# Optimization experiments

Measured on AMD Instinct MI355X. Metric: run time of the kernel, lower is better.

Reference implementation:

```python
import jax, jax.numpy as jnp
import numpy as np

B, T, I, H = 4096, 128, 32, 64


def _u(key, shape, bound):
    return jax.random.uniform(key, shape, jnp.float32, -bound, bound)


def setup_inputs() -> dict:
    key = jax.random.key(0)
    ks = jax.random.split(key, 14)
    bound = 1.0 / np.sqrt(H)  # torch LSTM/Linear default init scale
    inp = {
        "x": jax.random.normal(ks[0], (B, T, I), jnp.float32),
        "Wih0": _u(ks[1], (4 * H, I), bound),
        "Whh0": _u(ks[2], (4 * H, H), bound),
        "bih0": _u(ks[3], (4 * H,), bound),
        "bhh0": _u(ks[4], (4 * H,), bound),
        "Wih1": _u(ks[5], (4 * H, H), bound),
        "Whh1": _u(ks[6], (4 * H, H), bound),
        "bih1": _u(ks[7], (4 * H,), bound),
        "bhh1": _u(ks[8], (4 * H,), bound),
        "Wc1": _u(ks[9], (32, H), 1.0 / np.sqrt(H)),
        "bc1": _u(ks[10], (32,), 1.0 / np.sqrt(H)),
        "Wc2": _u(ks[11], (1, 32), 1.0 / np.sqrt(32)),
        "bc2": _u(ks[12], (1,), 1.0 / np.sqrt(32)),
    }
    return inp


def lstm_layer(x_tbi, Wih, Whh, bih, bhh):
    """x_tbi: [T, B, in]. Returns (all hidden [T,B,H], final hidden [B,H]).
    PyTorch gate order: i, f, g, o."""
    b = x_tbi.shape[1]
    h0 = jnp.zeros((b, Whh.shape[1]), x_tbi.dtype)
    c0 = jnp.zeros_like(h0)
    # precompute input projections for all timesteps in one big GEMM
    xproj = jnp.einsum('tbi,gi->tbg', x_tbi, Wih) + (bih + bhh)

    def step(carry, xp_t):
        h, c = carry
        gates = xp_t + h @ Whh.T  # [B, 4H]
        i, f, g, o = jnp.split(gates, 4, axis=-1)
        c = jax.nn.sigmoid(f) * c + jax.nn.sigmoid(i) * jnp.tanh(g)
        h = jax.nn.sigmoid(o) * jnp.tanh(c)
        return (h, c), h

    (hT, _), hs = jax.lax.scan(step, (h0, c0), xproj)
    return hs, hT


def reference(x, Wih0, Whh0, bih0, bhh0, Wih1, Whh1, bih1, bhh1, Wc1, bc1, Wc2, bc2):
    x_tbi = jnp.transpose(x, (1, 0, 2))  # [T, B, I]
    hs0, _ = lstm_layer(x_tbi, Wih0, Whh0, bih0, bhh0)
    # dropout between layers is identity in eval mode
    _, hT = lstm_layer(hs0, Wih1, Whh1, bih1, bhh1)  # h_n[-1]: [B, H]
    hidden = jax.nn.relu(hT @ Wc1.T + bc1)  # [B, 32]; classifier dropout = identity (eval)
    out = hidden @ Wc2.T + bc2  # [B, 1]
    return out.squeeze(-1)  # [B]
```

## Files before the change

### kernel.cpp

```cpp
#include <hip/hip_runtime.h>


#define TT 128
#define II 32
#define HH 64

typedef _Float16 half8 __attribute__((ext_vector_type(8)));
typedef float floatx4 __attribute__((ext_vector_type(4)));

__device__ __forceinline__ float fsig(float x) {
    return __builtin_amdgcn_rcpf(1.0f + __expf(-x));
}
__device__ __forceinline__ float ftanhf(float x) {
    return 1.0f - 2.0f * __builtin_amdgcn_rcpf(1.0f + __expf(2.0f * x));
}

__device__ __forceinline__ half8 load_w_frag(const float* __restrict__ W, int n, int K, int k0) {
    const float* p = W + (size_t)n * K + k0;
    float4 a = *(const float4*)p;
    float4 b = *(const float4*)(p + 4);
    half8 h;
    h[0] = (_Float16)a.x; h[1] = (_Float16)a.y; h[2] = (_Float16)a.z; h[3] = (_Float16)a.w;
    h[4] = (_Float16)b.x; h[5] = (_Float16)b.y; h[6] = (_Float16)b.z; h[7] = (_Float16)b.w;
    return h;
}

__global__ __launch_bounds__(512, 2) void lstm_fused(
    const float* __restrict__ x,
    const float* __restrict__ Wih0, const float* __restrict__ Whh0,
    const float* __restrict__ bih0, const float* __restrict__ bhh0,
    const float* __restrict__ Wih1, const float* __restrict__ Whh1,
    const float* __restrict__ bih1, const float* __restrict__ bhh1,
    const float* __restrict__ Wc1, const float* __restrict__ bc1,
    const float* __restrict__ Wc2, const float* __restrict__ bc2,
    float* __restrict__ out)
{
    __shared__ __align__(16) _Float16 xs[16][40];
    __shared__ __align__(16) _Float16 h0s[16][72];
    __shared__ __align__(16) _Float16 h1s[16][72];
    __shared__ __align__(16) float h1f[16][68];
    __shared__ float hid[16][32];

    const int tid  = threadIdx.x;
    const int wid  = tid >> 6;
    const int w4   = wid & 3;
    const bool isL0 = (wid < 4);
    const int lane = tid & 63;
    const int q  = lane >> 4;
    const int lr = lane & 15;
    const int b0 = blockIdx.x * 16;

    half8 bx0[4], bh0[4][2];
    half8 bi1[4][2], bh1[4][2];
    float biasv[4];
    if (isL0) {
        #pragma unroll
        for (int g = 0; g < 4; ++g) {
            int n = (w4 + 4 * g) * 16 + lr;
            bx0[g]    = load_w_frag(Wih0, n, 32, q * 8);
            bh0[g][0] = load_w_frag(Whh0, n, 64, q * 8);
            bh0[g][1] = load_w_frag(Whh0, n, 64, 32 + q * 8);
            biasv[g]  = bih0[n] + bhh0[n];
        }
    } else {
        #pragma unroll
        for (int g = 0; g < 4; ++g) {
            int n = (w4 + 4 * g) * 16 + lr;
            bi1[g][0] = load_w_frag(Wih1, n, 64, q * 8);
            bi1[g][1] = load_w_frag(Wih1, n, 64, 32 + q * 8);
            bh1[g][0] = load_w_frag(Whh1, n, 64, q * 8);
            bh1[g][1] = load_w_frag(Whh1, n, 64, 32 + q * 8);
            biasv[g]  = bih1[n] + bhh1[n];
        }
    }

    for (int i = tid; i < 16 * 72; i += 512) {
        ((_Float16*)h0s)[i] = (_Float16)0.0f;
        ((_Float16*)h1s)[i] = (_Float16)0.0f;
    }

    float cr[4] = {0.f, 0.f, 0.f, 0.f};

    const int xm = (tid >> 4) & 15;
    const int xf = (tid & 15) * 2;
    const float* xrow = x + ((size_t)(b0 + xm) * TT) * II + xf;
    float2 xbuf = {0.f, 0.f};
    if (isL0) {
        float2 x0 = *(const float2*)(xrow);
        xs[xm][xf]     = (_Float16)x0.x;
        xs[xm][xf + 1] = (_Float16)x0.y;
        if (TT > 1) xbuf = *(const float2*)(xrow + 1 * II);
    }

    for (int k = 0; k <= TT; ++k) {
        __syncthreads();

        const bool doL0 = isL0 && (k < TT);
        const bool doL1 = (!isL0) && (k >= 1);
        float hnew[4];
        float2 xnew = xbuf;

        if (doL0) {
            half8 xfrag = *(const half8*)&xs[lr][q * 8];
            half8 h0a   = *(const half8*)&h0s[lr][q * 8];
            half8 h0b   = *(const half8*)&h0s[lr][32 + q * 8];
            if (k + 2 < TT) xnew = *(const float2*)(xrow + (size_t)(k + 2) * II);
            floatx4 a0[4];
            #pragma unroll
            for (int g = 0; g < 4; ++g) {
                floatx4 accA = {biasv[g], biasv[g], biasv[g], biasv[g]};
                floatx4 z = {0.f, 0.f, 0.f, 0.f};
                accA = __builtin_amdgcn_mfma_f32_16x16x32_f16(xfrag, bx0[g],    accA, 0, 0, 0);
                accA = __builtin_amdgcn_mfma_f32_16x16x32_f16(h0a,   bh0[g][0], accA, 0, 0, 0);
                floatx4 accB = __builtin_amdgcn_mfma_f32_16x16x32_f16(h0b, bh0[g][1], z, 0, 0, 0);
                a0[g] = accA + accB;
            }
            #pragma unroll
            for (int r = 0; r < 4; ++r) {
                float ig = fsig(a0[0][r]);
                float fg = fsig(a0[1][r]);
                float gg = ftanhf(a0[2][r]);
                float og = fsig(a0[3][r]);
                float c = fg * cr[r] + ig * gg;
                cr[r] = c;
                hnew[r] = og * ftanhf(c);
            }
        }
        if (doL1) {
            half8 g0a = *(const half8*)&h0s[lr][q * 8];
            half8 g0b = *(const half8*)&h0s[lr][32 + q * 8];
            half8 h1a = *(const half8*)&h1s[lr][q * 8];
            half8 h1b = *(const half8*)&h1s[lr][32 + q * 8];
            floatx4 a1[4];
            #pragma unroll
            for (int g = 0; g < 4; ++g) {
                floatx4 accA = {biasv[g], biasv[g], biasv[g], biasv[g]};
                floatx4 z = {0.f, 0.f, 0.f, 0.f};
                accA = __builtin_amdgcn_mfma_f32_16x16x32_f16(g0a, bi1[g][0], accA, 0, 0, 0);
                accA = __builtin_amdgcn_mfma_f32_16x16x32_f16(g0b, bi1[g][1], accA, 0, 0, 0);
                floatx4 accB = __builtin_amdgcn_mfma_f32_16x16x32_f16(h1a, bh1[g][0], z,    0, 0, 0);
                accB         = __builtin_amdgcn_mfma_f32_16x16x32_f16(h1b, bh1[g][1], accB, 0, 0, 0);
                a1[g] = accA + accB;
            }
            #pragma unroll
            for (int r = 0; r < 4; ++r) {
                float ig = fsig(a1[0][r]);
                float fg = fsig(a1[1][r]);
                float gg = ftanhf(a1[2][r]);
                float og = fsig(a1[3][r]);
                float c = fg * cr[r] + ig * gg;
                cr[r] = c;
                hnew[r] = og * ftanhf(c);
            }
        }

        __syncthreads();

        if (doL0) {
            #pragma unroll
            for (int r = 0; r < 4; ++r)
                h0s[q * 4 + r][w4 * 16 + lr] = (_Float16)hnew[r];
            if (k + 1 < TT) {
                xs[xm][xf]     = (_Float16)xbuf.x;
                xs[xm][xf + 1] = (_Float16)xbuf.y;
            }
            xbuf = xnew;
        }
        if (doL1) {
            if (k == TT) {
                #pragma unroll
                for (int r = 0; r < 4; ++r)
                    h1f[q * 4 + r][w4 * 16 + lr] = hnew[r];
            } else {
                #pragma unroll
                for (int r = 0; r < 4; ++r)
                    h1s[q * 4 + r][w4 * 16 + lr] = (_Float16)hnew[r];
            }
        }
    }
    __syncthreads();

    if (tid < 256) {
        int m = tid >> 4;
        int u = (tid & 15) * 2;
        float a = bc1[u], b = bc1[u + 1];
        const float* w0 = Wc1 + u * 64;
        const float* w1 = Wc1 + (u + 1) * 64;
        #pragma unroll 8
        for (int kk = 0; kk < 64; ++kk) {
            float hv = h1f[m][kk];
            a += hv * w0[kk];
            b += hv * w1[kk];
        }
        hid[m][u]     = fmaxf(a, 0.f);
        hid[m][u + 1] = fmaxf(b, 0.f);
    }
    __syncthreads();
    if (tid < 16) {
        float o = bc2[0];
        #pragma unroll
        for (int u = 0; u < 32; ++u) o += hid[tid][u] * Wc2[u];
        out[b0 + tid] = o;
    }
}

extern "C" void kernel_launch(void* const* d_in, const int* in_sizes, int n_in,
                              void* d_out, int out_size, void* d_ws, size_t ws_size,
                              hipStream_t stream) {
    (void)in_sizes; (void)n_in; (void)d_ws; (void)ws_size; (void)out_size;
    const float* x    = (const float*)d_in[0];
    const float* Wih0 = (const float*)d_in[1];
    const float* Whh0 = (const float*)d_in[2];
    const float* bih0 = (const float*)d_in[3];
    const float* bhh0 = (const float*)d_in[4];
    const float* Wih1 = (const float*)d_in[5];
    const float* Whh1 = (const float*)d_in[6];
    const float* bih1 = (const float*)d_in[7];
    const float* bhh1 = (const float*)d_in[8];
    const float* Wc1  = (const float*)d_in[9];
    const float* bc1  = (const float*)d_in[10];
    const float* Wc2  = (const float*)d_in[11];
    const float* bc2  = (const float*)d_in[12];
    lstm_fused<<<dim3(256), dim3(512), 0, stream>>>(
        x, Wih0, Whh0, bih0, bhh0, Wih1, Whh1, bih1, bhh1, Wc1, bc1, Wc2, bc2,
        (float*)d_out);
}
```

Measured before the change: 226.5 us.

## Double-buffer LDS hidden state to drop a barrier and fuse gate activations

Hidden state and x tiles in LDS become ping-pong buffers indexed by step parity, so each timestep needs one __syncthreads instead of two. Gate activations are rewritten to use exp2 directly, and sigmoid(a)*tanh(b) is fused into a single reciprocal with clamping. MFMA accumulation is chained into one accumulator instead of two summed partial chains. The goal is to cut barrier stalls and transcendental count on the serial recurrence, at the cost of more LDS and a longer dependent MFMA chain.

```diff
diff --git a/kernel.cpp b/kernel.cpp
--- a/kernel.cpp
+++ b/kernel.cpp
@@ -8,12 +8,7 @@
 typedef _Float16 half8 __attribute__((ext_vector_type(8)));
 typedef float floatx4 __attribute__((ext_vector_type(4)));
 
-__device__ __forceinline__ float fsig(float x) {
-    return __builtin_amdgcn_rcpf(1.0f + __expf(-x));
-}
-__device__ __forceinline__ float ftanhf(float x) {
-    return 1.0f - 2.0f * __builtin_amdgcn_rcpf(1.0f + __expf(2.0f * x));
-}
+#define LOG2E 1.4426950408889634f
 
 __device__ __forceinline__ half8 load_w_frag(const float* __restrict__ W, int n, int K, int k0) {
     const float* p = W + (size_t)n * K + k0;
@@ -23,6 +18,20 @@
     h[0] = (_Float16)a.x; h[1] = (_Float16)a.y; h[2] = (_Float16)a.z; h[3] = (_Float16)a.w;
     h[4] = (_Float16)b.x; h[5] = (_Float16)b.y; h[6] = (_Float16)b.z; h[7] = (_Float16)b.w;
     return h;
+}
+
+__device__ __forceinline__ float sig_tanh(float a, float b) {
+    float bb = fminf(fmaxf(b, -15.f), 15.f);
+    float u  = __builtin_amdgcn_exp2f(bb * (2.0f * LOG2E));
+    float v  = __builtin_amdgcn_exp2f(-a * LOG2E);
+    float num = u - 1.0f;
+    float d1  = u + 1.0f;
+    float den = fmaf(v, d1, d1);
+    return num * __builtin_amdgcn_rcpf(den);
+}
+
+__device__ __forceinline__ float fsig(float x) {
+    return __builtin_amdgcn_rcpf(1.0f + __builtin_amdgcn_exp2f(-x * LOG2E));
 }
 
 __global__ __launch_bounds__(512, 2) void lstm_fused(
@@ -35,9 +44,9 @@
     const float* __restrict__ Wc2, const float* __restrict__ bc2,
     float* __restrict__ out)
 {
-    __shared__ __align__(16) _Float16 xs[16][40];
-    __shared__ __align__(16) _Float16 h0s[16][72];
-    __shared__ __align__(16) _Float16 h1s[16][72];
+    __shared__ __align__(16) _Float16 xs[2][16][40];
+    __shared__ __align__(16) _Float16 h0s[2][16][72];
+    __shared__ __align__(16) _Float16 h1s[2][16][72];
     __shared__ __align__(16) float h1f[16][68];
     __shared__ float hid[16][32];
 
@@ -74,7 +83,7 @@
         }
     }
 
-    for (int i = tid; i < 16 * 72; i += 512) {
+    for (int i = tid; i < 2 * 16 * 72; i += 512) {
         ((_Float16*)h0s)[i] = (_Float16)0.0f;
         ((_Float16*)h1s)[i] = (_Float16)0.0f;
     }
@@ -87,82 +96,74 @@
     float2 xbuf = {0.f, 0.f};
     if (isL0) {
         float2 x0 = *(const float2*)(xrow);
-        xs[xm][xf]     = (_Float16)x0.x;
-        xs[xm][xf + 1] = (_Float16)x0.y;
+        xs[0][xm][xf]     = (_Float16)x0.x;
+        xs[0][xm][xf + 1] = (_Float16)x0.y;
         if (TT > 1) xbuf = *(const float2*)(xrow + 1 * II);
     }
 
     for (int k = 0; k <= TT; ++k) {
         __syncthreads();
 
+        const int rd = (k + 1) & 1;
+        const int wr = k & 1;
         const bool doL0 = isL0 && (k < TT);
         const bool doL1 = (!isL0) && (k >= 1);
         float hnew[4];
         float2 xnew = xbuf;
 
         if (doL0) {
-            half8 xfrag = *(const half8*)&xs[lr][q * 8];
-            half8 h0a   = *(const half8*)&h0s[lr][q * 8];
-            half8 h0b   = *(const half8*)&h0s[lr][32 + q * 8];
+            half8 xfrag = *(const half8*)&xs[wr][lr][q * 8];
+            half8 h0a   = *(const half8*)&h0s[rd][lr][q * 8];
+            half8 h0b   = *(const half8*)&h0s[rd][lr][32 + q * 8];
             if (k + 2 < TT) xnew = *(const float2*)(xrow + (size_t)(k + 2) * II);
             floatx4 a0[4];
             #pragma unroll
             for (int g = 0; g < 4; ++g) {
-                floatx4 accA = {biasv[g], biasv[g], biasv[g], biasv[g]};
-                floatx4 z = {0.f, 0.f, 0.f, 0.f};
-                accA = __builtin_amdgcn_mfma_f32_16x16x32_f16(xfrag, bx0[g],    accA, 0, 0, 0);
-                accA = __builtin_amdgcn_mfma_f32_16x16x32_f16(h0a,   bh0[g][0], accA, 0, 0, 0);
-                floatx4 accB = __builtin_amdgcn_mfma_f32_16x16x32_f16(h0b, bh0[g][1], z, 0, 0, 0);
-                a0[g] = accA + accB;
+                floatx4 acc = {biasv[g], biasv[g], biasv[g], biasv[g]};
+                acc = __builtin_amdgcn_mfma_f32_16x16x32_f16(xfrag, bx0[g],    acc, 0, 0, 0);
+                acc = __builtin_amdgcn_mfma_f32_16x16x32_f16(h0a,   bh0[g][0], acc, 0, 0, 0);
+                acc = __builtin_amdgcn_mfma_f32_16x16x32_f16(h0b,   bh0[g][1], acc, 0, 0, 0);
+                a0[g] = acc;
             }
             #pragma unroll
             for (int r = 0; r < 4; ++r) {
-                float ig = fsig(a0[0][r]);
-                float fg = fsig(a0[1][r]);
-                float gg = ftanhf(a0[2][r]);
-                float og = fsig(a0[3][r]);
-                float c = fg * cr[r] + ig * gg;
+                float sf = fsig(a0[1][r]);
+                float c  = fmaf(sf, cr[r], sig_tanh(a0[0][r], a0[2][r]));
                 cr[r] = c;
-                hnew[r] = og * ftanhf(c);
+                hnew[r] = sig_tanh(a0[3][r], c);
             }
         }
         if (doL1) {
-            half8 g0a = *(const half8*)&h0s[lr][q * 8];
-            half8 g0b = *(const half8*)&h0s[lr][32 + q * 8];
-            half8 h1a = *(const half8*)&h1s[lr][q * 8];
-            half8 h1b = *(const half8*)&h1s[lr][32 + q * 8];
+            half8 g0a = *(const half8*)&h0s[rd][lr][q * 8];
+            half8 g0b = *(const half8*)&h0s[rd][lr][32 + q * 8];
+            half8 h1a = *(const half8*)&h1s[rd][lr][q * 8];
+            half8 h1b = *(const half8*)&h1s[rd][lr][32 + q * 8];
             floatx4 a1[4];
             #pragma unroll
             for (int g = 0; g < 4; ++g) {
-                floatx4 accA = {biasv[g], biasv[g], biasv[g], biasv[g]};
-                floatx4 z = {0.f, 0.f, 0.f, 0.f};
-                accA = __builtin_amdgcn_mfma_f32_16x16x32_f16(g0a, bi1[g][0], accA, 0, 0, 0);
-                accA = __builtin_amdgcn_mfma_f32_16x16x32_f16(g0b, bi1[g][1], accA, 0, 0, 0);
-                floatx4 accB = __builtin_amdgcn_mfma_f32_16x16x32_f16(h1a, bh1[g][0], z,    0, 0, 0);
-                accB         = __builtin_amdgcn_mfma_f32_16x16x32_f16(h1b, bh1[g][1], accB, 0, 0, 0);
-                a1[g] = accA + accB;
+                floatx4 acc = {biasv[g], biasv[g], biasv[g], biasv[g]};
+                acc = __builtin_amdgcn_mfma_f32_16x16x32_f16(g0a, bi1[g][0], acc, 0, 0, 0);
+                acc = __builtin_amdgcn_mfma_f32_16x16x32_f16(g0b, bi1[g][1], acc, 0, 0, 0);
+                acc = __builtin_amdgcn_mfma_f32_16x16x32_f16(h1a, bh1[g][0], acc, 0, 0, 0);
+                acc = __builtin_amdgcn_mfma_f32_16x16x32_f16(h1b, bh1[g][1], acc, 0, 0, 0);
+                a1[g] = acc;
             }
             #pragma unroll
             for (int r = 0; r < 4; ++r) {
-                float ig = fsig(a1[0][r]);
-                float fg = fsig(a1[1][r]);
-                float gg = ftanhf(a1[2][r]);
-                float og = fsig(a1[3][r]);
-                float c = fg * cr[r] + ig * gg;
+                float sf = fsig(a1[1][r]);
+                float c  = fmaf(sf, cr[r], sig_tanh(a1[0][r], a1[2][r]));
                 cr[r] = c;
-                hnew[r] = og * ftanhf(c);
-            }
-        }
-
-        __syncthreads();
+                hnew[r] = sig_tanh(a1[3][r], c);
+            }
+        }
 
         if (doL0) {
             #pragma unroll
             for (int r = 0; r < 4; ++r)
-                h0s[q * 4 + r][w4 * 16 + lr] = (_Float16)hnew[r];
+                h0s[wr][q * 4 + r][w4 * 16 + lr] = (_Float16)hnew[r];
             if (k + 1 < TT) {
-                xs[xm][xf]     = (_Float16)xbuf.x;
-                xs[xm][xf + 1] = (_Float16)xbuf.y;
+                xs[rd][xm][xf]     = (_Float16)xbuf.x;
+                xs[rd][xm][xf + 1] = (_Float16)xbuf.y;
             }
             xbuf = xnew;
         }
@@ -174,7 +175,7 @@
             } else {
                 #pragma unroll
                 for (int r = 0; r < 4; ++r)
-                    h1s[q * 4 + r][w4 * 16 + lr] = (_Float16)hnew[r];
+                    h1s[wr][q * 4 + r][w4 * 16 + lr] = (_Float16)hnew[r];
             }
         }
     }
```

Result: faster. 206.0 us (-9.1%).
